# Kernel optimization log

Measured on AMD Instinct MI355X. Metric: run time of the kernel, lower is better.

## Reference

```python
import jax, jax.numpy as jnp
import numpy as np

N = 100000          # buses
E = 200000          # branch edges (avg degree 2, power grid)
IN_DIM = 6          # x[:, 4:10]
EDGE_DIM = 4
HID = 32
OUT_DIM = 2


def _nnconv(x_in, src, dst, edge_attr, w1, b1, w2, b2, root, bias):
    """PyG NNConv (aggr='add', root_weight=True, bias=True)."""
    in_c, out_c = root.shape
    # edge-conditioned weight matrices: [E, in_c, out_c]
    h = jax.nn.relu(edge_attr @ w1 + b1)
    W = (h @ w2 + b2).reshape(-1, in_c, out_c)
    # gather source features, per-edge matvec, scatter-add to targets
    msg = jnp.einsum('ei,eio->eo', x_in[src], W)           # [E, out_c]
    agg = jax.ops.segment_sum(msg, dst, num_segments=x_in.shape[0])
    return agg + x_in @ root + bias


def setup_inputs() -> dict:
    key = jax.random.key(0)
    ks = jax.random.split(key, 8)
    inp = {
        'x': jax.random.normal(ks[0], (N, 10), dtype=jnp.float32),
        'edge_index': jax.random.randint(ks[1], (2, E), 0, N, dtype=jnp.int64),
        'edge_attr': jax.random.normal(ks[2], (E, EDGE_DIM), dtype=jnp.float32),
    }
    dims = [(IN_DIM, HID), (HID, HID), (HID, HID), (HID, OUT_DIM)]
    s = 0.1
    for i, (ic, oc) in enumerate(dims):
        k = jax.random.split(ks[3 + i], 3)
        inp[f'w1_{i}'] = jax.random.normal(k[0], (EDGE_DIM, HID), dtype=jnp.float32) * s
        inp[f'b1_{i}'] = jnp.zeros((HID,), dtype=jnp.float32)
        inp[f'w2_{i}'] = jax.random.normal(k[1], (HID, ic * oc), dtype=jnp.float32) * s
        inp[f'b2_{i}'] = jnp.zeros((ic * oc,), dtype=jnp.float32)
        inp[f'root_{i}'] = jax.random.normal(k[2], (ic, oc), dtype=jnp.float32) * s
        inp[f'bias_{i}'] = jnp.zeros((oc,), dtype=jnp.float32)
    return inp


def reference(x, edge_index, edge_attr,
              w1_0, b1_0, w2_0, b2_0, root_0, bias_0,
              w1_1, b1_1, w2_1, b2_1, root_1, bias_1,
              w1_2, b1_2, w2_2, b2_2, root_2, bias_2,
              w1_3, b1_3, w2_3, b2_3, root_3, bias_3):
    convs = [
        (w1_0, b1_0, w2_0, b2_0, root_0, bias_0),
        (w1_1, b1_1, w2_1, b2_1, root_1, bias_1),
        (w1_2, b1_2, w2_2, b2_2, root_2, bias_2),
        (w1_3, b1_3, w2_3, b2_3, root_3, bias_3),
    ]
    src, dst = edge_index[0], edge_index[1]
    h = x[:, 4:10]                                    # [N, 6]
    n_convs = len(convs)
    for i, p in enumerate(convs):
        h = _nnconv(h, src, dst, edge_attr, *p)
        if i < n_convs - 1:
            h = jax.nn.relu(h)
    return h
```

## Files before the change

### kernel.cpp

```cpp
#include <hip/hip_runtime.h>
#include <hip/hip_fp16.h>

typedef __attribute__((ext_vector_type(8)))  _Float16 half8v;
typedef __attribute__((ext_vector_type(16))) float    f32x16;

static constexpr int BSWZ_STEPS = 226;
static constexpr int BSWZ_TOT   = BSWZ_STEPS * 512;

struct Prm {
    const float* x;
    const float* w2[4]; const float* b2[4];
    const float* root[4]; const float* bias[4];
    _Float16* xin;
    _Float16* bswz;
    _Float16* aggz;
    float* outz;
    int N;
};

__global__ __launch_bounds__(256) void prep(Prm p, int NB8, int NZA, int NZO)
{
    int b = blockIdx.x;
    if (b < 452) {
        int i = b * 256 + threadIdx.x;
        int T = i >> 9, t2 = i & 511;
        int j = t2 & 7, l = (t2 >> 3) & 63;
        int g = l >> 5, o = l & 31;
        int layer, cls, t;
        if (T < 17)       { layer = 0; cls = 0; t = T; }
        else if (T < 19)  { layer = 0; cls = 1; t = T - 17; }
        else if (T < 85)  { layer = 1; cls = 0; t = T - 19; }
        else if (T < 88)  { layer = 1; cls = 1; t = T - 85; }
        else if (T < 154) { layer = 2; cls = 0; t = T - 88; }
        else if (T < 157) { layer = 2; cls = 1; t = T - 154; }
        else if (T < 223) { layer = 3; cls = 0; t = T - 157; }
        else              { layer = 3; cls = 1; t = T - 223; }
        const int INP   = (layer == 0) ? 8 : 32;
        const int IN_C  = (layer == 0) ? 6 : 32;
        const int OUT_C = (layer == 3) ? 2 : 32;
        float v = 0.f;
        if (cls == 0) {
            const int S_MAIN = 2 * INP;
            if (t < S_MAIN) {
                int kap = 16 * t + 8 * g + j;
                int k  = (INP == 8) ? (kap >> 3) : (kap >> 5);
                int ii = (INP == 8) ? (kap & 7)  : (kap & 31);
                if (ii < IN_C && o < OUT_C)
                    v = p.w2[layer][(size_t)k * (IN_C * OUT_C) + ii * OUT_C + o];
            } else {
                int ii = 16 * (t - S_MAIN) + 8 * g + j;
                if (ii < IN_C && o < OUT_C)
                    v = p.b2[layer][ii * OUT_C + o];
            }
        } else {
            const int nroot = (layer == 0) ? 1 : 2;
            if (t < nroot) {
                int ii = 16 * t + 8 * g + j;
                if (ii < IN_C && o < OUT_C)
                    v = p.root[layer][ii * OUT_C + o];
            } else {
                if (g == 0 && j == 0 && o < OUT_C)
                    v = p.bias[layer][o];
            }
        }
        p.bswz[i] = (_Float16)v;
    } else if (b < 452 + NB8) {
        int i = (b - 452) * 256 + threadIdx.x;
        if (i < p.N * 8) {
            int v = i >> 3, c = i & 7;
            float val = (c < 6) ? p.x[(size_t)v * 10 + 4 + c] : 0.f;
            p.xin[i] = (_Float16)val;
        }
    } else if (b < 452 + NB8 + NZA) {
        long long i = (long long)(b - 452 - NB8) * 256 + threadIdx.x;
        if (i < (long long)p.N * 12)
            ((uint4*)p.aggz)[i] = uint4{0u, 0u, 0u, 0u};
    } else {
        int v = (b - 452 - NB8 - NZA) * 256 + threadIdx.x;
        if (v < p.N)
            ((float2*)p.outz)[v] = float2{0.f, 0.f};
    }
}

static __device__ __forceinline__ void gather32h(
    const _Float16* __restrict__ fprev, int s, int g, half8v& xh0, half8v& xh1)
{
    const half8v* fp = (const half8v*)(fprev + (size_t)s * 32);
    xh0 = fp[g];
    xh1 = fp[2 + g];
    #pragma unroll
    for (int j = 0; j < 8; ++j) {
        xh0[j] = xh0[j] > (_Float16)0.f ? xh0[j] : (_Float16)0.f;
        xh1[j] = xh1[j] > (_Float16)0.f ? xh1[j] : (_Float16)0.f;
    }
}

static __device__ __forceinline__ void pk_atomic_row(
    _Float16* __restrict__ aggH, int row, int o, float mine)
{
    float oth = __shfl_xor(mine, 1);
    if ((o & 1) == 0 && row >= 0) {
        __half2 v = __floats2half2_rn(mine, oth);
        unsafeAtomicAdd((__half2*)aggH + (((size_t)row << 5) + o) / 2, v);
    }
}

template<int INP, int OUT_C>
__global__ __launch_bounds__(512) void edge(
    const _Float16* __restrict__ xin,
    const _Float16* __restrict__ fprev,
    const int*      __restrict__ src,
    const int*      __restrict__ dst,
    const float*    __restrict__ ea,
    const float*    __restrict__ w1,
    const float*    __restrict__ b1,
    const _Float16* __restrict__ bAll,
    _Float16* __restrict__ aggH,
    float*    __restrict__ aggF,
    int E, int N, int ntileE, int ntot)
{
    constexpr int NREAL = (INP == 32) ? 66 : 17;
    constexpr int NSELF = (INP == 32) ? 3  : 2;
    constexpr int NSTEP = NREAL + NSELF;

    __shared__ half8v ldsb[NSTEP * 64];
    {
        const half8v* bp = (const half8v*)bAll;
        for (int i = threadIdx.x; i < NSTEP * 64; i += 512)
            ldsb[i] = bp[i];
    }
    __syncthreads();

    const int lane = threadIdx.x & 63;
    const int g = lane >> 5, o = lane & 31;
    const int lrow = lane & 31;
    const int wv = (blockIdx.x * 512 + threadIdx.x) >> 6;
    const int nw = gridDim.x * 8;

    half8v ones;
    #pragma unroll
    for (int j = 0; j < 8; ++j) ones[j] = (_Float16)0.f;
    ones[0] = (_Float16)1.f;

    for (int tile = wv; tile < ntot; tile += nw) {
        f32x16 C;
        #pragma unroll
        for (int i = 0; i < 16; ++i) C[i] = 0.f;

        if (tile < ntileE) {
            const int e0 = tile * 32;
            const int er = e0 + lrow;
            const int ec = er < E ? er : (E - 1);
            const int s  = src[ec];
            const float4 av = *(const float4*)(ea + 4ll * ec);

            half8v xh0, xh1;
            if constexpr (INP == 32) gather32h(fprev, s, g, xh0, xh1);
            else                     xh0 = *(const half8v*)(xin + (size_t)s * 8);

            if constexpr (INP == 32) {
                #pragma unroll 4
                for (int k = 0; k < 32; ++k) {
                    half8v bf0 = ldsb[(2*k    ) * 64 + lane];
                    half8v bf1 = ldsb[(2*k + 1) * 64 + lane];
                    float hk = fmaf(av.x, w1[k], b1[k]);
                    hk = fmaf(av.y, w1[32 + k], hk);
                    hk = fmaf(av.z, w1[64 + k], hk);
                    hk = fmaf(av.w, w1[96 + k], hk);
                    hk = fmaxf(hk, 0.f);
                    const _Float16 hh = (_Float16)hk;
                    half8v hs;
                    #pragma unroll
                    for (int j = 0; j < 8; ++j) hs[j] = hh;
                    C = __builtin_amdgcn_mfma_f32_32x32x16_f16(hs * xh0, bf0, C, 0, 0, 0);
                    C = __builtin_amdgcn_mfma_f32_32x32x16_f16(hs * xh1, bf1, C, 0, 0, 0);
                }
                C = __builtin_amdgcn_mfma_f32_32x32x16_f16(xh0, ldsb[64*64 + lane], C, 0, 0, 0);
                C = __builtin_amdgcn_mfma_f32_32x32x16_f16(xh1, ldsb[65*64 + lane], C, 0, 0, 0);
            } else {
                #pragma unroll 4
                for (int t = 0; t < 16; ++t) {
                    half8v bf = ldsb[t * 64 + lane];
                    const int k = 2 * t + g;
                    float hk = fmaf(av.x, w1[k], b1[k]);
                    hk = fmaf(av.y, w1[32 + k], hk);
                    hk = fmaf(av.z, w1[64 + k], hk);
                    hk = fmaf(av.w, w1[96 + k], hk);
                    hk = fmaxf(hk, 0.f);
                    const _Float16 hh = (_Float16)hk;
                    half8v hs;
                    #pragma unroll
                    for (int j = 0; j < 8; ++j) hs[j] = hh;
                    C = __builtin_amdgcn_mfma_f32_32x32x16_f16(hs * xh0, bf, C, 0, 0, 0);
                }
                half8v zz;
                #pragma unroll
                for (int j = 0; j < 8; ++j) zz[j] = (_Float16)0.f;
                half8v a = (g == 0) ? xh0 : zz;
                C = __builtin_amdgcn_mfma_f32_32x32x16_f16(a, ldsb[16*64 + lane], C, 0, 0, 0);
            }

            if constexpr (OUT_C == 32) {
                #pragma unroll
                for (int q = 0; q < 4; ++q) {
                    const int eb = e0 + 8 * q + 4 * g;
                    int rows[4];
                    if (eb + 3 < E) {
                        const int4 dd = *(const int4*)(dst + eb);
                        rows[0] = dd.x; rows[1] = dd.y; rows[2] = dd.z; rows[3] = dd.w;
                    } else {
                        #pragma unroll
                        for (int m = 0; m < 4; ++m)
                            rows[m] = (eb + m < E) ? dst[eb + m] : -1;
                    }
                    #pragma unroll
                    for (int m = 0; m < 4; ++m)
                        pk_atomic_row(aggH, rows[m], o, C[4*q + m]);
                }
            } else {
                if (o < OUT_C) {
                    #pragma unroll
                    for (int q = 0; q < 4; ++q) {
                        const int eb = e0 + 8 * q + 4 * g;
                        #pragma unroll
                        for (int m = 0; m < 4; ++m)
                            if (eb + m < E)
                                unsafeAtomicAdd(aggF + (size_t)dst[eb + m] * OUT_C + o,
                                                C[4*q + m]);
                    }
                }
            }
        } else {
            const int v0 = (tile - ntileE) * 32;
            const int vr = v0 + lrow;
            const int vc = vr < N ? vr : (N - 1);

            if constexpr (INP == 32) {
                half8v xh0, xh1;
                gather32h(fprev, vc, g, xh0, xh1);
                C = __builtin_amdgcn_mfma_f32_32x32x16_f16(xh0,  ldsb[(NREAL+0)*64 + lane], C, 0, 0, 0);
                C = __builtin_amdgcn_mfma_f32_32x32x16_f16(xh1,  ldsb[(NREAL+1)*64 + lane], C, 0, 0, 0);
                C = __builtin_amdgcn_mfma_f32_32x32x16_f16(ones, ldsb[(NREAL+2)*64 + lane], C, 0, 0, 0);
            } else {
                half8v xh0 = *(const half8v*)(xin + (size_t)vc * 8);
                C = __builtin_amdgcn_mfma_f32_32x32x16_f16(xh0,  ldsb[(NREAL+0)*64 + lane], C, 0, 0, 0);
                C = __builtin_amdgcn_mfma_f32_32x32x16_f16(ones, ldsb[(NREAL+1)*64 + lane], C, 0, 0, 0);
            }

            if constexpr (OUT_C == 32) {
                #pragma unroll
                for (int q = 0; q < 4; ++q) {
                    #pragma unroll
                    for (int m = 0; m < 4; ++m) {
                        const int row = v0 + 8*q + 4*g + m;
                        pk_atomic_row(aggH, row < N ? row : -1, o, C[4*q + m]);
                    }
                }
            } else {
                if (o < OUT_C) {
                    #pragma unroll
                    for (int q = 0; q < 4; ++q) {
                        #pragma unroll
                        for (int m = 0; m < 4; ++m) {
                            const int row = v0 + 8*q + 4*g + m;
                            if (row < N)
                                unsafeAtomicAdd(aggF + (size_t)row * OUT_C + o, C[4*q + m]);
                        }
                    }
                }
            }
        }
    }
}

extern "C" void kernel_launch(void* const* d_in, const int* in_sizes, int n_in,
                              void* d_out, int out_size, void* d_ws, size_t ws_size,
                              hipStream_t stream)
{
    const float* x  = (const float*)d_in[0];
    const int*   ei = (const int*)d_in[1];
    const float* ea = (const float*)d_in[2];

    const int E = in_sizes[2] / 4;
    const int N = in_sizes[0] / 10;
    const int* src = ei;
    const int* dst = ei + E;

    const float* p[4][6];
    for (int L = 0; L < 4; ++L)
        for (int j = 0; j < 6; ++j)
            p[L][j] = (const float*)d_in[3 + 6 * L + j];

    char* w = (char*)d_ws;
    auto carve = [&](size_t bytes) {
        char* q = w; w += (bytes + 255) & ~(size_t)255; return (void*)q;
    };
    _Float16* xin  = (_Float16*)carve((size_t)N * 8 * 2);
    _Float16* aggz = (_Float16*)carve((size_t)3 * N * 32 * 2);
    _Float16* bswz = (_Float16*)carve((size_t)BSWZ_TOT * 2);
    _Float16* agg0 = aggz;
    _Float16* agg1 = aggz + (size_t)N * 32;
    _Float16* agg2 = aggz + (size_t)2 * N * 32;
    float* out  = (float*)d_out;

    Prm prm{};
    prm.x = x;
    for (int L = 0; L < 4; ++L) {
        prm.w2[L] = p[L][2]; prm.b2[L] = p[L][3];
        prm.root[L] = p[L][4]; prm.bias[L] = p[L][5];
    }
    prm.xin = xin; prm.bswz = bswz; prm.aggz = aggz; prm.outz = out; prm.N = N;

    const int NB8 = (N * 8 + 255) / 256;
    const int NZA = (N * 12 + 255) / 256;
    const int NZO = (N + 255) / 256;

    const int ntileE = (E + 31) / 32;
    const int ntileN = (N + 31) / 32;
    const int ntot   = ntileE + ntileN;
    int NB = (ntot + 7) / 8;
    if (NB > 512) NB = 512;

    prep<<<452 + NB8 + NZA + NZO, 256, 0, stream>>>(prm, NB8, NZA, NZO);

    edge<8, 32><<<NB, 512, 0, stream>>>(
        xin, nullptr, src, dst, ea, p[0][0], p[0][1],
        bswz + 0 * 512, agg0, nullptr, E, N, ntileE, ntot);

    edge<32, 32><<<NB, 512, 0, stream>>>(
        nullptr, agg0, src, dst, ea, p[1][0], p[1][1],
        bswz + 19 * 512, agg1, nullptr, E, N, ntileE, ntot);

    edge<32, 32><<<NB, 512, 0, stream>>>(
        nullptr, agg1, src, dst, ea, p[2][0], p[2][1],
        bswz + 88 * 512, agg2, nullptr, E, N, ntileE, ntot);

    edge<32, 2><<<NB, 512, 0, stream>>>(
        nullptr, agg2, src, dst, ea, p[3][0], p[3][1],
        bswz + 157 * 512, nullptr, out, E, N, ntileE, ntot);
}
```

Baseline: 126.6 us.

## Replace atomic scatter-add with CSR sort by destination and segmented sum

Builds a CSR ordering of edges by destination (histogram, two-pass scan, scatter of src and edge_attr), then has the edge kernels write per-edge messages to a buffer. A separate segsum kernel per layer reduces the messages per node and also applies the root and bias terms in fp32, which removes the fp16 atomics and the zero-init of the aggregation buffers. In exchange it adds five preprocessing kernels with their own atomics, four extra launches, and an E×32 fp16 message buffer that is written and read back each layer.

```diff
diff --git a/kernel.cpp b/kernel.cpp
--- a/kernel.cpp
+++ b/kernel.cpp
@@ -4,82 +4,130 @@
 typedef __attribute__((ext_vector_type(8)))  _Float16 half8v;
 typedef __attribute__((ext_vector_type(16))) float    f32x16;
 
-static constexpr int BSWZ_STEPS = 226;
+static constexpr int BSWZ_STEPS = 215;
 static constexpr int BSWZ_TOT   = BSWZ_STEPS * 512;
 
 struct Prm {
     const float* x;
     const float* w2[4]; const float* b2[4];
-    const float* root[4]; const float* bias[4];
     _Float16* xin;
     _Float16* bswz;
-    _Float16* aggz;
-    float* outz;
+    int* cnt;
     int N;
 };
 
-__global__ __launch_bounds__(256) void prep(Prm p, int NB8, int NZA, int NZO)
+__global__ __launch_bounds__(256) void prep(Prm p, int NB8, int NBC)
 {
     int b = blockIdx.x;
-    if (b < 452) {
+    if (b < 430) {
         int i = b * 256 + threadIdx.x;
         int T = i >> 9, t2 = i & 511;
         int j = t2 & 7, l = (t2 >> 3) & 63;
         int g = l >> 5, o = l & 31;
-        int layer, cls, t;
-        if (T < 17)       { layer = 0; cls = 0; t = T; }
-        else if (T < 19)  { layer = 0; cls = 1; t = T - 17; }
-        else if (T < 85)  { layer = 1; cls = 0; t = T - 19; }
-        else if (T < 88)  { layer = 1; cls = 1; t = T - 85; }
-        else if (T < 154) { layer = 2; cls = 0; t = T - 88; }
-        else if (T < 157) { layer = 2; cls = 1; t = T - 154; }
-        else if (T < 223) { layer = 3; cls = 0; t = T - 157; }
-        else              { layer = 3; cls = 1; t = T - 223; }
+        int layer, t;
+        if (T < 17)       { layer = 0; t = T; }
+        else if (T < 83)  { layer = 1; t = T - 17; }
+        else if (T < 149) { layer = 2; t = T - 83; }
+        else              { layer = 3; t = T - 149; }
         const int INP   = (layer == 0) ? 8 : 32;
         const int IN_C  = (layer == 0) ? 6 : 32;
         const int OUT_C = (layer == 3) ? 2 : 32;
+        const int S_MAIN = 2 * INP;
         float v = 0.f;
-        if (cls == 0) {
-            const int S_MAIN = 2 * INP;
-            if (t < S_MAIN) {
-                int kap = 16 * t + 8 * g + j;
-                int k  = (INP == 8) ? (kap >> 3) : (kap >> 5);
-                int ii = (INP == 8) ? (kap & 7)  : (kap & 31);
-                if (ii < IN_C && o < OUT_C)
-                    v = p.w2[layer][(size_t)k * (IN_C * OUT_C) + ii * OUT_C + o];
-            } else {
-                int ii = 16 * (t - S_MAIN) + 8 * g + j;
-                if (ii < IN_C && o < OUT_C)
-                    v = p.b2[layer][ii * OUT_C + o];
-            }
+        if (t < S_MAIN) {
+            int kap = 16 * t + 8 * g + j;
+            int k  = (INP == 8) ? (kap >> 3) : (kap >> 5);
+            int ii = (INP == 8) ? (kap & 7)  : (kap & 31);
+            if (ii < IN_C && o < OUT_C)
+                v = p.w2[layer][(size_t)k * (IN_C * OUT_C) + ii * OUT_C + o];
         } else {
-            const int nroot = (layer == 0) ? 1 : 2;
-            if (t < nroot) {
-                int ii = 16 * t + 8 * g + j;
-                if (ii < IN_C && o < OUT_C)
-                    v = p.root[layer][ii * OUT_C + o];
-            } else {
-                if (g == 0 && j == 0 && o < OUT_C)
-                    v = p.bias[layer][o];
-            }
+            int ii = 16 * (t - S_MAIN) + 8 * g + j;
+            if (ii < IN_C && o < OUT_C)
+                v = p.b2[layer][ii * OUT_C + o];
         }
         p.bswz[i] = (_Float16)v;
-    } else if (b < 452 + NB8) {
-        int i = (b - 452) * 256 + threadIdx.x;
+    } else if (b < 430 + NB8) {
+        int i = (b - 430) * 256 + threadIdx.x;
         if (i < p.N * 8) {
             int v = i >> 3, c = i & 7;
             float val = (c < 6) ? p.x[(size_t)v * 10 + 4 + c] : 0.f;
             p.xin[i] = (_Float16)val;
         }
-    } else if (b < 452 + NB8 + NZA) {
-        long long i = (long long)(b - 452 - NB8) * 256 + threadIdx.x;
-        if (i < (long long)p.N * 12)
-            ((uint4*)p.aggz)[i] = uint4{0u, 0u, 0u, 0u};
     } else {
-        int v = (b - 452 - NB8 - NZA) * 256 + threadIdx.x;
-        if (v < p.N)
-            ((float2*)p.outz)[v] = float2{0.f, 0.f};
-    }
+        int i = (b - 430 - NB8) * 256 + threadIdx.x;
+        if (i < p.N) p.cnt[i] = 0;
+    }
+}
+
+__global__ __launch_bounds__(256) void hist(
+    const int* __restrict__ dst, int* __restrict__ cnt, int E)
+{
+    int e = blockIdx.x * 256 + threadIdx.x;
+    if (e < E) atomicAdd(&cnt[dst[e]], 1);
+}
+
+__global__ __launch_bounds__(256) void scan_part(
+    const int* __restrict__ cnt, int* __restrict__ bsum, int N)
+{
+    __shared__ int lds[256];
+    int i = blockIdx.x * 256 + threadIdx.x;
+    int v = (i < N) ? cnt[i] : 0;
+    lds[threadIdx.x] = v;
+    __syncthreads();
+    #pragma unroll
+    for (int off = 128; off > 0; off >>= 1) {
+        if (threadIdx.x < off) lds[threadIdx.x] += lds[threadIdx.x + off];
+        __syncthreads();
+    }
+    if (threadIdx.x == 0) bsum[blockIdx.x] = lds[0];
+}
+
+__global__ __launch_bounds__(256) void scan_final(
+    int* __restrict__ cnt, const int* __restrict__ bsum,
+    int* __restrict__ rowptr, int N)
+{
+    __shared__ int lds[256];
+    __shared__ int pref;
+    const int b = blockIdx.x;
+    int s = 0;
+    for (int j = threadIdx.x; j < b; j += 256) s += bsum[j];
+    lds[threadIdx.x] = s;
+    __syncthreads();
+    #pragma unroll
+    for (int off = 128; off > 0; off >>= 1) {
+        if (threadIdx.x < off) lds[threadIdx.x] += lds[threadIdx.x + off];
+        __syncthreads();
+    }
+    if (threadIdx.x == 0) pref = lds[0];
+    __syncthreads();
+    int i = (b << 8) + threadIdx.x;
+    int v = (i < N) ? cnt[i] : 0;
+    lds[threadIdx.x] = v;
+    __syncthreads();
+    for (int off = 1; off < 256; off <<= 1) {
+        int u = (threadIdx.x >= off) ? lds[threadIdx.x - off] : 0;
+        __syncthreads();
+        lds[threadIdx.x] += u;
+        __syncthreads();
+    }
+    int excl = lds[threadIdx.x] - v + pref;
+    if (i < N) {
+        rowptr[i] = excl;
+        cnt[i] = excl;
+        if (i == N - 1) rowptr[N] = excl + v;
+    }
+}
+
+__global__ __launch_bounds__(256) void scatter(
+    const int* __restrict__ src, const int* __restrict__ dst,
+    const float* __restrict__ ea, int* __restrict__ cursor,
+    int* __restrict__ srcP, float* __restrict__ eaP, int E)
+{
+    int e = blockIdx.x * 256 + threadIdx.x;
+    if (e >= E) return;
+    int pos = atomicAdd(&cursor[dst[e]], 1);
+    srcP[pos] = src[e];
+    ((float4*)eaP)[pos] = ((const float4*)ea)[e];
 }
 
 static __device__ __forceinline__ void gather32h(
@@ -95,33 +143,19 @@
     }
 }
 
-static __device__ __forceinline__ void pk_atomic_row(
-    _Float16* __restrict__ aggH, int row, int o, float mine)
-{
-    float oth = __shfl_xor(mine, 1);
-    if ((o & 1) == 0 && row >= 0) {
-        __half2 v = __floats2half2_rn(mine, oth);
-        unsafeAtomicAdd((__half2*)aggH + (((size_t)row << 5) + o) / 2, v);
-    }
-}
-
 template<int INP, int OUT_C>
 __global__ __launch_bounds__(512) void edge(
     const _Float16* __restrict__ xin,
     const _Float16* __restrict__ fprev,
-    const int*      __restrict__ src,
-    const int*      __restrict__ dst,
-    const float*    __restrict__ ea,
+    const int*      __restrict__ srcP,
+    const float*    __restrict__ eaP,
     const float*    __restrict__ w1,
     const float*    __restrict__ b1,
     const _Float16* __restrict__ bAll,
-    _Float16* __restrict__ aggH,
-    float*    __restrict__ aggF,
-    int E, int N, int ntileE, int ntot)
-{
-    constexpr int NREAL = (INP == 32) ? 66 : 17;
-    constexpr int NSELF = (INP == 32) ? 3  : 2;
-    constexpr int NSTEP = NREAL + NSELF;
+    _Float16* __restrict__ msg,
+    int E, int ntileE)
+{
+    constexpr int NSTEP = (INP == 32) ? 66 : 17;
 
     __shared__ half8v ldsb[NSTEP * 64];
     {
@@ -137,139 +171,153 @@
     const int wv = (blockIdx.x * 512 + threadIdx.x) >> 6;
     const int nw = gridDim.x * 8;
 
-    half8v ones;
-    #pragma unroll
-    for (int j = 0; j < 8; ++j) ones[j] = (_Float16)0.f;
-    ones[0] = (_Float16)1.f;
-
-    for (int tile = wv; tile < ntot; tile += nw) {
+    for (int tile = wv; tile < ntileE; tile += nw) {
+        const int e0 = tile * 32;
+        const int er = e0 + lrow;
+        const int ec = er < E ? er : (E - 1);
+        const int s  = srcP[ec];
+        const float4 av = *(const float4*)(eaP + 4ll * ec);
+
+        half8v xh0, xh1;
+        if constexpr (INP == 32) gather32h(fprev, s, g, xh0, xh1);
+        else                     xh0 = *(const half8v*)(xin + (size_t)s * 8);
+
         f32x16 C;
         #pragma unroll
         for (int i = 0; i < 16; ++i) C[i] = 0.f;
 
-        if (tile < ntileE) {
-            const int e0 = tile * 32;
-            const int er = e0 + lrow;
-            const int ec = er < E ? er : (E - 1);
-            const int s  = src[ec];
-            const float4 av = *(const float4*)(ea + 4ll * ec);
-
-            half8v xh0, xh1;
-            if constexpr (INP == 32) gather32h(fprev, s, g, xh0, xh1);
-            else                     xh0 = *(const half8v*)(xin + (size_t)s * 8);
-
-            if constexpr (INP == 32) {
-                #pragma unroll 4
-                for (int k = 0; k < 32; ++k) {
-                    half8v bf0 = ldsb[(2*k    ) * 64 + lane];
-                    half8v bf1 = ldsb[(2*k + 1) * 64 + lane];
-                    float hk = fmaf(av.x, w1[k], b1[k]);
-                    hk = fmaf(av.y, w1[32 + k], hk);
-                    hk = fmaf(av.z, w1[64 + k], hk);
-                    hk = fmaf(av.w, w1[96 + k], hk);
-                    hk = fmaxf(hk, 0.f);
-                    const _Float16 hh = (_Float16)hk;
-                    half8v hs;
-                    #pragma unroll
-                    for (int j = 0; j < 8; ++j) hs[j] = hh;
-                    C = __builtin_amdgcn_mfma_f32_32x32x16_f16(hs * xh0, bf0, C, 0, 0, 0);
-                    C = __builtin_amdgcn_mfma_f32_32x32x16_f16(hs * xh1, bf1, C, 0, 0, 0);
-                }
-                C = __builtin_amdgcn_mfma_f32_32x32x16_f16(xh0, ldsb[64*64 + lane], C, 0, 0, 0);
-                C = __builtin_amdgcn_mfma_f32_32x32x16_f16(xh1, ldsb[65*64 + lane], C, 0, 0, 0);
-            } else {
-                #pragma unroll 4
-                for (int t = 0; t < 16; ++t) {
-                    half8v bf = ldsb[t * 64 + lane];
-                    const int k = 2 * t + g;
-                    float hk = fmaf(av.x, w1[k], b1[k]);
-                    hk = fmaf(av.y, w1[32 + k], hk);
-                    hk = fmaf(av.z, w1[64 + k], hk);
-                    hk = fmaf(av.w, w1[96 + k], hk);
-                    hk = fmaxf(hk, 0.f);
-                    const _Float16 hh = (_Float16)hk;
-                    half8v hs;
-                    #pragma unroll
-                    for (int j = 0; j < 8; ++j) hs[j] = hh;
-                    C = __builtin_amdgcn_mfma_f32_32x32x16_f16(hs * xh0, bf, C, 0, 0, 0);
-                }
-                half8v zz;
+        if constexpr (INP == 32) {
+            #pragma unroll 4
+            for (int k = 0; k < 32; ++k) {
+                half8v bf0 = ldsb[(2*k    ) * 64 + lane];
+                half8v bf1 = ldsb[(2*k + 1) * 64 + lane];
+                float hk = fmaf(av.x, w1[k], b1[k]);
+                hk = fmaf(av.y, w1[32 + k], hk);
+                hk = fmaf(av.z, w1[64 + k], hk);
+                hk = fmaf(av.w, w1[96 + k], hk);
+                hk = fmaxf(hk, 0.f);
+                const _Float16 hh = (_Float16)hk;
+                half8v hs;
                 #pragma unroll
-                for (int j = 0; j < 8; ++j) zz[j] = (_Float16)0.f;
-                half8v a = (g == 0) ? xh0 : zz;
-                C = __builtin_amdgcn_mfma_f32_32x32x16_f16(a, ldsb[16*64 + lane], C, 0, 0, 0);
+                for (int j = 0; j < 8; ++j) hs[j] = hh;
+                C = __builtin_amdgcn_mfma_f32_32x32x16_f16(hs * xh0, bf0, C, 0, 0, 0);
+                C = __builtin_amdgcn_mfma_f32_32x32x16_f16(hs * xh1, bf1, C, 0, 0, 0);
             }
-
-            if constexpr (OUT_C == 32) {
+            C = __builtin_amdgcn_mfma_f32_32x32x16_f16(xh0, ldsb[64*64 + lane], C, 0, 0, 0);
+            C = __builtin_amdgcn_mfma_f32_32x32x16_f16(xh1, ldsb[65*64 + lane], C, 0, 0, 0);
+        } else {
+            #pragma unroll 4
+            for (int t = 0; t < 16; ++t) {
+                half8v bf = ldsb[t * 64 + lane];
+                const int k = 2 * t + g;
+                float hk = fmaf(av.x, w1[k], b1[k]);
+                hk = fmaf(av.y, w1[32 + k], hk);
+                hk = fmaf(av.z, w1[64 + k], hk);
+                hk = fmaf(av.w, w1[96 + k], hk);
+                hk = fmaxf(hk, 0.f);
+                const _Float16 hh = (_Float16)hk;
+                half8v hs;
                 #pragma unroll
-                for (int q = 0; q < 4; ++q) {
-                    const int eb = e0 + 8 * q + 4 * g;
-                    int rows[4];
-                    if (eb + 3 < E) {
-                        const int4 dd = *(const int4*)(dst + eb);
-                        rows[0] = dd.x; rows[1] = dd.y; rows[2] = dd.z; rows[3] = dd.w;
-                    } else {
-                        #pragma unroll
-                        for (int m = 0; m < 4; ++m)
-                            rows[m] = (eb + m < E) ? dst[eb + m] : -1;
-                    }
-                    #pragma unroll
-                    for (int m = 0; m < 4; ++m)
-                        pk_atomic_row(aggH, rows[m], o, C[4*q + m]);
-                }
-            } else {
-                if (o < OUT_C) {
-                    #pragma unroll
-                    for (int q = 0; q < 4; ++q) {
-                        const int eb = e0 + 8 * q + 4 * g;
-                        #pragma unroll
-                        for (int m = 0; m < 4; ++m)
-                            if (eb + m < E)
-                                unsafeAtomicAdd(aggF + (size_t)dst[eb + m] * OUT_C + o,
-                                                C[4*q + m]);
-                    }
+                for (int j = 0; j < 8; ++j) hs[j] = hh;
+                C = __builtin_amdgcn_mfma_f32_32x32x16_f16(hs * xh0, bf, C, 0, 0, 0);
+            }
+            half8v zz;
+            #pragma unroll
+            for (int j = 0; j < 8; ++j) zz[j] = (_Float16)0.f;
+            half8v a = (g == 0) ? xh0 : zz;
+            C = __builtin_amdgcn_mfma_f32_32x32x16_f16(a, ldsb[16*64 + lane], C, 0, 0, 0);
+        }
+
+        const bool full = (e0 + 31 < E);
+        #pragma unroll
+        for (int q = 0; q < 4; ++q) {
+            #pragma unroll
+            for (int m = 0; m < 4; ++m) {
+                const int row = e0 + 8*q + 4*g + m;
+                float mine = C[4*q + m];
+                float oth  = __shfl_xor(mine, 1);
+                if constexpr (OUT_C == 32) {
+                    if (!(o & 1) && (full || row < E))
+                        *(__half2*)(msg + (size_t)row * 32 + o) =
+                            __floats2half2_rn(mine, oth);
+                } else {
+                    if (o == 0 && (full || row < E))
+                        *(__half2*)(msg + (size_t)row * 2) =
+                            __floats2half2_rn(mine, oth);
                 }
             }
+        }
+    }
+}
+
+template<int IN_C, int OUT_C>
+__global__ __launch_bounds__(256) void segsum(
+    const _Float16* __restrict__ fprev,
+    const _Float16* __restrict__ msg,
+    const int*      __restrict__ rowptr,
+    const float*    __restrict__ root,
+    const float*    __restrict__ bias,
+    _Float16* __restrict__ aggOut,
+    float*    __restrict__ outF,
+    int N)
+{
+    constexpr int CH = (OUT_C >= 8) ? 8 : OUT_C;
+    constexpr int NC = OUT_C / CH;
+    int tid = blockIdx.x * 256 + threadIdx.x;
+    int v = tid / NC, c = tid % NC;
+    if (v >= N) return;
+    const int c0 = c * CH;
+
+    float acc[CH];
+    #pragma unroll
+    for (int j = 0; j < CH; ++j) acc[j] = bias[c0 + j];
+
+    if constexpr (IN_C == 6) {
+        half8v u = *(const half8v*)(fprev + (size_t)v * 8);
+        #pragma unroll
+        for (int i = 0; i < 6; ++i) {
+            float xi = (float)u[i];
+            #pragma unroll
+            for (int j = 0; j < CH; ++j)
+                acc[j] = fmaf(xi, root[i * OUT_C + c0 + j], acc[j]);
+        }
+    } else {
+        const half8v* fp = (const half8v*)(fprev + (size_t)v * 32);
+        #pragma unroll
+        for (int blk = 0; blk < 4; ++blk) {
+            half8v u = fp[blk];
+            #pragma unroll
+            for (int jj = 0; jj < 8; ++jj) {
+                float xi = fmaxf((float)u[jj], 0.f);
+                int i = blk * 8 + jj;
+                #pragma unroll
+                for (int j = 0; j < CH; ++j)
+                    acc[j] = fmaf(xi, root[i * OUT_C + c0 + j], acc[j]);
+            }
+        }
+    }
+
+    const int r1 = rowptr[v + 1];
+    for (int r = rowptr[v]; r < r1; ++r) {
+        if constexpr (OUT_C == 32) {
+            half8v u = *(const half8v*)(msg + (size_t)r * 32 + c0);
+            #pragma unroll
+            for (int j = 0; j < CH; ++j) acc[j] += (float)u[j];
         } else {
-            const int v0 = (tile - ntileE) * 32;
-            const int vr = v0 + lrow;
-            const int vc = vr < N ? vr : (N - 1);
-
-            if constexpr (INP == 32) {
-                half8v xh0, xh1;
-                gather32h(fprev, vc, g, xh0, xh1);
-                C = __builtin_amdgcn_mfma_f32_32x32x16_f16(xh0,  ldsb[(NREAL+0)*64 + lane], C, 0, 0, 0);
-                C = __builtin_amdgcn_mfma_f32_32x32x16_f16(xh1,  ldsb[(NREAL+1)*64 + lane], C, 0, 0, 0);
-                C = __builtin_amdgcn_mfma_f32_32x32x16_f16(ones, ldsb[(NREAL+2)*64 + lane], C, 0, 0, 0);
-            } else {
-                half8v xh0 = *(const half8v*)(xin + (size_t)vc * 8);
-                C = __builtin_amdgcn_mfma_f32_32x32x16_f16(xh0,  ldsb[(NREAL+0)*64 + lane], C, 0, 0, 0);
-                C = __builtin_amdgcn_mfma_f32_32x32x16_f16(ones, ldsb[(NREAL+1)*64 + lane], C, 0, 0, 0);
-            }
-
-            if constexpr (OUT_C == 32) {
-                #pragma unroll
-                for (int q = 0; q < 4; ++q) {
-                    #pragma unroll
-                    for (int m = 0; m < 4; ++m) {
-                        const int row = v0 + 8*q + 4*g + m;
-                        pk_atomic_row(aggH, row < N ? row : -1, o, C[4*q + m]);
-                    }
-                }
-            } else {
-                if (o < OUT_C) {
-                    #pragma unroll
-                    for (int q = 0; q < 4; ++q) {
-                        #pragma unroll
-                        for (int m = 0; m < 4; ++m) {
-                            const int row = v0 + 8*q + 4*g + m;
-                            if (row < N)
-                                unsafeAtomicAdd(aggF + (size_t)row * OUT_C + o, C[4*q + m]);
-                        }
-                    }
-                }
-            }
-        }
+            __half2 u = *(const __half2*)(msg + (size_t)r * 2);
+            float2 f = __half22float2(u);
+            acc[0] += f.x; acc[1] += f.y;
+        }
+    }
+
+    if constexpr (OUT_C == 32) {
+        half8v u;
+        #pragma unroll
+        for (int j = 0; j < CH; ++j) u[j] = (_Float16)acc[j];
+        *(half8v*)(aggOut + (size_t)v * 32 + c0) = u;
+    } else {
+        float2 o2; o2.x = acc[0]; o2.y = acc[1];
+        ((float2*)outF)[v] = o2;
     }
 }
 
@@ -295,47 +343,55 @@
     auto carve = [&](size_t bytes) {
         char* q = w; w += (bytes + 255) & ~(size_t)255; return (void*)q;
     };
-    _Float16* xin  = (_Float16*)carve((size_t)N * 8 * 2);
-    _Float16* aggz = (_Float16*)carve((size_t)3 * N * 32 * 2);
-    _Float16* bswz = (_Float16*)carve((size_t)BSWZ_TOT * 2);
-    _Float16* agg0 = aggz;
-    _Float16* agg1 = aggz + (size_t)N * 32;
-    _Float16* agg2 = aggz + (size_t)2 * N * 32;
-    float* out  = (float*)d_out;
+    _Float16* xin   = (_Float16*)carve((size_t)N * 8 * 2);
+    _Float16* aggA  = (_Float16*)carve((size_t)N * 32 * 2);
+    _Float16* aggB  = (_Float16*)carve((size_t)N * 32 * 2);
+    _Float16* msg   = (_Float16*)carve((size_t)E * 32 * 2);
+    float*    eaP   = (float*)carve((size_t)E * 4 * 4);
+    int*      srcP  = (int*)carve((size_t)E * 4);
+    int*      rowptr= (int*)carve((size_t)(N + 1) * 4);
+    int*      cnt   = (int*)carve((size_t)N * 4);
+    int*      bsum  = (int*)carve(4096);
+    _Float16* bswz  = (_Float16*)carve((size_t)BSWZ_TOT * 2);
+    float* out = (float*)d_out;
 
     Prm prm{};
     prm.x = x;
-    for (int L = 0; L < 4; ++L) {
-        prm.w2[L] = p[L][2]; prm.b2[L] = p[L][3];
-        prm.root[L] = p[L][4]; prm.bias[L] = p[L][5];
-    }
-    prm.xin = xin; prm.bswz = bswz; prm.aggz = aggz; prm.outz = out; prm.N = N;
+    for (int L = 0; L < 4; ++L) { prm.w2[L] = p[L][2]; prm.b2[L] = p[L][3]; }
+    prm.xin = xin; prm.bswz = bswz; prm.cnt = cnt; prm.N = N;
 
     const int NB8 = (N * 8 + 255) / 256;
-    const int NZA = (N * 12 + 255) / 256;
-    const int NZO = (N + 255) / 256;
+    const int NBC = (N + 255) / 256;
+    const int EBK = (E + 255) / 256;
 
     const int ntileE = (E + 31) / 32;
-    const int ntileN = (N + 31) / 32;
-    const int ntot   = ntileE + ntileN;
-    int NB = (ntot + 7) / 8;
-    if (NB > 512) NB = 512;
-
-    prep<<<452 + NB8 + NZA + NZO, 256, 0, stream>>>(prm, NB8, NZA, NZO);
-
-    edge<8, 32><<<NB, 512, 0, stream>>>(
-        xin, nullptr, src, dst, ea, p[0][0], p[0][1],
-        bswz + 0 * 512, agg0, nullptr, E, N, ntileE, ntot);
-
-    edge<32, 32><<<NB, 512, 0, stream>>>(
-        nullptr, agg0, src, dst, ea, p[1][0], p[1][1],
-        bswz + 19 * 512, agg1, nullptr, E, N, ntileE, ntot);
-
-    edge<32, 32><<<NB, 512, 0, stream>>>(
-        nullptr, agg1, src, dst, ea, p[2][0], p[2][1],
-        bswz + 88 * 512, agg2, nullptr, E, N, ntileE, ntot);
-
-    edge<32, 2><<<NB, 512, 0, stream>>>(
-        nullptr, agg2, src, dst, ea, p[3][0], p[3][1],
-        bswz + 157 * 512, nullptr, out, E, N, ntileE, ntot);
-}
+    int NBE = (ntileE + 7) / 8;
+    const int NBS32 = (N * 4 + 255) / 256;
+    const int NBS2  = NBC;
+
+    prep      <<<430 + NB8 + NBC, 256, 0, stream>>>(prm, NB8, NBC);
+    hist      <<<EBK, 256, 0, stream>>>(dst, cnt, E);
+    scan_part <<<NBC, 256, 0, stream>>>(cnt, bsum, N);
+    scan_final<<<NBC, 256, 0, stream>>>(cnt, bsum, rowptr, N);
+    scatter   <<<EBK, 256, 0, stream>>>(src, dst, ea, cnt, srcP, eaP, E);
+
+    edge<8, 32><<<NBE, 512, 0, stream>>>(
+        xin, nullptr, srcP, eaP, p[0][0], p[0][1], bswz + 0 * 512, msg, E, ntileE);
+    segsum<6, 32><<<NBS32, 256, 0, stream>>>(
+        xin, msg, rowptr, p[0][4], p[0][5], aggA, nullptr, N);
+
+    edge<32, 32><<<NBE, 512, 0, stream>>>(
+        nullptr, aggA, srcP, eaP, p[1][0], p[1][1], bswz + 17 * 512, msg, E, ntileE);
+    segsum<32, 32><<<NBS32, 256, 0, stream>>>(
+        aggA, msg, rowptr, p[1][4], p[1][5], aggB, nullptr, N);
+
+    edge<32, 32><<<NBE, 512, 0, stream>>>(
+        nullptr, aggB, srcP, eaP, p[2][0], p[2][1], bswz + 83 * 512, msg, E, ntileE);
+    segsum<32, 32><<<NBS32, 256, 0, stream>>>(
+        aggB, msg, rowptr, p[2][4], p[2][5], aggA, nullptr, N);
+
+    edge<32, 2><<<NBE, 512, 0, stream>>>(
+        nullptr, aggA, srcP, eaP, p[3][0], p[3][1], bswz + 149 * 512, msg, E, ntileE);
+    segsum<32, 2><<<NBS2, 256, 0, stream>>>(
+        aggA, msg, rowptr, p[3][4], p[3][5], nullptr, out, N);
+}
```

Result: slower. 175.7 us (+38.8%).
